# Performance work log

Hardware: AMD Instinct MI355X
Metric: run time of the kernel (lower is better)

The kernel has to match this reference:

```python
import jax, jax.numpy as jnp
import numpy as np

DN = ('NCHW', 'OIHW', 'NCHW')


def conv(x, w, s, p):
    return jax.lax.conv_general_dilated(x, w, (s, s), [(p, p), (p, p)], dimension_numbers=DN)


def batchnorm(x, g, b, eps=1e-5):
    # torch BatchNorm2d in training mode: biased batch stats over (N,H,W)
    mu = jnp.mean(x, (0, 2, 3), keepdims=True)
    var = jnp.var(x, (0, 2, 3), keepdims=True)
    return (x - mu) * jax.lax.rsqrt(var + eps) * g.reshape(1, -1, 1, 1) + b.reshape(1, -1, 1, 1)


def pconv(x, mask, W, b, s, p, gb, act):
    # PartialConvLayer.forward
    k = W.shape[-1]
    y = conv(x * mask, W, s, p)
    mc = conv(mask, jnp.ones((1, 1, k, k), x.dtype), s, p)  # all-ones mask conv (frozen)
    zero = mc == 0
    msum = jnp.where(zero, 1.0, mc)
    if b is not None:
        bias = b.reshape(1, -1, 1, 1)
        y = (y - bias) / msum + bias
    else:
        y = y / msum
    y = jnp.where(zero, 0.0, y)
    new_mask = jnp.where(zero, 0.0, 1.0).astype(x.dtype)
    if gb is not None:
        y = batchnorm(y, gb[0], gb[1])
    if act == 'relu':
        y = jax.nn.relu(y)
    elif act == 'leaky':
        y = jnp.where(y >= 0, y, 0.2 * y)
    return y, new_mask


def nlm(mask, feat, h2):
    # Vectorized batch_NLM: Nadaraya-Watson estimator between miss and bkg pixels.
    # Equivalent to the original triple loop: for each miss pixel i,
    #   out[i] = sum_j exp(-||x_i-x_j||^2/h^2) x_j / sum_j exp(-...)   over bkg j.
    # Subtracting the per-row min distance before exp is mathematically identical
    # (the factor cancels in the ratio) and numerically stable.
    bs, C, H, W = feat.shape
    N = H * W
    x = feat.transpose(0, 2, 3, 1).reshape(bs, N, C)
    bkg = mask.reshape(bs, N) > 0.5
    sq = jnp.sum(x * x, -1)  # [bs,N]
    D = jnp.maximum(sq[:, :, None] + sq[:, None, :] - 2.0 * jnp.einsum('bic,bjc->bij', x, x), 0.0)
    Dm = jnp.where(bkg[:, None, :], D, jnp.inf)
    dmin = jnp.min(Dm, -1, keepdims=True)
    w = jnp.where(bkg[:, None, :], jnp.exp(-(D - dmin) / h2), 0.0)
    avg = jnp.einsum('bij,bjc->bic', w, x) / jnp.sum(w, -1, keepdims=True)
    out = jnp.where(bkg[:, :, None], x, avg)  # only miss pixels are replaced
    return out.reshape(bs, H, W, C).transpose(0, 3, 1, 2)


def up2(x):
    return jnp.repeat(jnp.repeat(x, 2, axis=2), 2, axis=3)


def forward(input_x, mask, enc1_W, enc2_W, enc3_W, enc4_W, dec4_W, dec3_W, dec2_W, dec1_W, dec1_b,
            enc2_g, enc2_b, enc3_g, enc3_b, enc4_g, enc4_b,
            dec4_g, dec4_b, dec3_g, dec3_b, dec2_g, dec2_b):
    H_GAUSS2 = 25.0  # h_gaussian = 5
    h0, m0 = input_x, mask
    h1, m1 = pconv(h0, m0, enc1_W, None, 2, 3, None, 'relu')                 # down-7, bn=False
    h2, m2 = pconv(h1, m1, enc2_W, None, 2, 2, (enc2_g, enc2_b), 'relu')     # down-5
    # NLM feature swapping at layer 2 (torch code detaches -> stop_gradient)
    h2 = jax.lax.stop_gradient(nlm(m2, h2, H_GAUSS2))
    buffer_swapped = h2
    h3, m3 = pconv(h2, m2, enc3_W, None, 2, 1, (enc3_g, enc3_b), 'relu')     # down-3
    h4, m4 = pconv(h3, m3, enc4_W, None, 2, 1, (enc4_g, enc4_b), 'relu')     # down-3

    out, omask = h4, m4
    out, omask = up2(out), up2(omask)
    out, omask = pconv(jnp.concatenate([out, h3], 1), omask, dec4_W, None, 1, 1, (dec4_g, dec4_b), 'leaky')
    out, omask = up2(out), up2(omask)
    out, omask = pconv(jnp.concatenate([out, buffer_swapped], 1), omask, dec3_W, None, 1, 1, (dec3_g, dec3_b), 'leaky')
    out, omask = up2(out), up2(omask)
    out, omask = pconv(jnp.concatenate([out, h1], 1), omask, dec2_W, None, 1, 1, (dec2_g, dec2_b), 'leaky')
    out, omask = up2(out), up2(omask)
    out, omask = pconv(jnp.concatenate([out, h0], 1), omask, dec1_W, dec1_b, 1, 1, None, 'none')  # bn=False, bias, no act
    return out


def setup_inputs() -> dict:
    key = jax.random.key(0)
    ks = jax.random.split(key, 12)

    def kaiming(k, shape):
        fan_in = shape[1] * shape[2] * shape[3]
        return jax.random.normal(k, shape, jnp.float32) * np.float32(np.sqrt(2.0 / fan_in))

    bs = 8
    input_x = jax.random.normal(ks[0], (bs, 128, 144, 144), jnp.float32)
    # mask: 1 = background (valid), 0 = missing. Hole large enough to survive two downsamples.
    mask = jnp.ones((bs, 1, 144, 144), jnp.float32).at[:, :, 40:96, 40:96].set(0.0)

    inp = {
        'input_x': input_x,
        'mask': mask,
        'enc1_W': kaiming(ks[1], (256, 128, 7, 7)),
        'enc2_W': kaiming(ks[2], (512, 256, 5, 5)),
        'enc3_W': kaiming(ks[3], (512, 512, 3, 3)),
        'enc4_W': kaiming(ks[4], (512, 512, 3, 3)),
        'dec4_W': kaiming(ks[5], (512, 1024, 3, 3)),
        'dec3_W': kaiming(ks[6], (512, 1024, 3, 3)),
        'dec2_W': kaiming(ks[7], (256, 768, 3, 3)),
        'dec1_W': kaiming(ks[8], (128, 384, 3, 3)),
        'dec1_b': jnp.zeros((128,), jnp.float32),
    }
    for name, c in [('enc2', 512), ('enc3', 512), ('enc4', 512), ('dec4', 512), ('dec3', 512), ('dec2', 256)]:
        inp[name + '_g'] = jnp.ones((c,), jnp.float32)
        inp[name + '_b'] = jnp.zeros((c,), jnp.float32)
    return inp


def reference(input_x, mask, enc1_W, enc2_W, enc3_W, enc4_W, dec4_W, dec3_W, dec2_W, dec1_W, dec1_b,
              enc2_g, enc2_b, enc3_g, enc3_b, enc4_g, enc4_b,
              dec4_g, dec4_b, dec3_g, dec3_b, dec2_g, dec2_b):
    return forward(input_x, mask, enc1_W, enc2_W, enc3_W, enc4_W, dec4_W, dec3_W, dec2_W, dec1_W, dec1_b,
                   enc2_g, enc2_b, enc3_g, enc3_b, enc4_g, enc4_b,
                   dec4_g, dec4_b, dec3_g, dec3_b, dec2_g, dec2_b)
```

## Files before the change

### kernel.cpp

```cpp
#include <hip/hip_runtime.h>
#include <math.h>

#define ACT_NONE 0
#define ACT_RELU 1
#define ACT_LEAKY 2

#define EPI_F32 0
#define EPI_PAIR_RELU 1
#define EPI_F32_BIAS 2

typedef __attribute__((ext_vector_type(8))) short short8;
typedef __attribute__((ext_vector_type(8))) __bf16 bf16x8;
typedef __attribute__((ext_vector_type(4))) float f32x4;
typedef __attribute__((ext_vector_type(4))) unsigned uint4v;

__device__ __forceinline__ float actf(float y, int act) {
    if (act == ACT_RELU)  return y > 0.f ? y : 0.f;
    if (act == ACT_LEAKY) return y >= 0.f ? y : 0.2f * y;
    return y;
}

__device__ __forceinline__ unsigned f2bf_rne(float f) {
    unsigned u = __float_as_uint(f);
    return (u + 0x7FFFu + ((u >> 16) & 1u)) >> 16;
}
__device__ __forceinline__ float bf2f(unsigned h) { return __uint_as_float(h << 16); }
__device__ __forceinline__ unsigned splitpack(float f) {
    unsigned hi = f2bf_rne(f);
    float r = f - bf2f(hi);
    unsigned lo = f2bf_rne(r);
    return (hi & 0xFFFFu) | (lo << 16);
}

__device__ __forceinline__ f32x4 mfma16(short8 a, short8 b, f32x4 c) {
    return __builtin_amdgcn_mfma_f32_16x16x32_bf16(
        __builtin_bit_cast(bf16x8, a), __builtin_bit_cast(bf16x8, b), c, 0, 0, 0);
}

template<int K, int S, bool MHALF>
__global__ void maskconv_kernel(const float* __restrict__ M, int HM, int WM,
                                float* __restrict__ mc, float* __restrict__ nm,
                                int N, int Hin, int Win, int Hout, int Wout) {
    constexpr int P = (K - 1) / 2;
    int idx = blockIdx.x * blockDim.x + threadIdx.x;
    int total = N * Hout * Wout;
    if (idx >= total) return;
    int wo = idx % Wout;
    int t  = idx / Wout;
    int ho = t % Hout;
    int n  = t / Hout;
    float s = 0.f;
    for (int kh = 0; kh < K; ++kh) {
        int ih = ho * S - P + kh;
        if ((unsigned)ih >= (unsigned)Hin) continue;
        const float* mrow = M + ((size_t)n * HM + (MHALF ? (ih >> 1) : ih)) * WM;
        for (int kw = 0; kw < K; ++kw) {
            int iw = wo * S - P + kw;
            if ((unsigned)iw < (unsigned)Win)
                s += mrow[MHALF ? (iw >> 1) : iw];
        }
    }
    mc[idx] = s;
    nm[idx] = (s == 0.f) ? 0.f : 1.f;
}

__global__ void wtransform(const float* __restrict__ W, short* __restrict__ Whi,
                           short* __restrict__ Wlo, int Cout, int Cin, int Ksz,
                           size_t total) {
    size_t idx = (size_t)blockIdx.x * blockDim.x + threadIdx.x;
    if (idx >= total) return;
    int j = (int)(idx & 7);
    int lane = (int)((idx >> 3) & 63);
    size_t r = idx >> 9;
    int COB = Cout >> 4, KB = Cin >> 5;
    int cob = (int)(r % COB); r /= COB;
    int kb = (int)(r % KB);
    int tap = (int)(r / KB);
    int co = cob * 16 + (lane & 15);
    int ci = kb * 32 + (lane >> 4) * 8 + j;
    float f = W[((size_t)co * Cin + ci) * Ksz + tap];
    unsigned hi = f2bf_rne(f);
    float rr = f - bf2f(hi);
    unsigned lo = f2bf_rne(rr);
    Whi[idx] = (short)hi;
    Wlo[idx] = (short)lo;
}

template<int K, int S, int TH, int TW, int NFW, bool AF32, int EPI>
__global__ __launch_bounds__(512) void conv_enc(
    const void* __restrict__ Asrc, int Cin, int Hin, int Win,
    const float* __restrict__ M,
    const short* __restrict__ Whi, const short* __restrict__ Wlo,
    const float* __restrict__ mc, const float* __restrict__ bias,
    void* __restrict__ outp,
    int Hout, int Wout, int Cout, int TX)
{
    constexpr int P = (K - 1) / 2;
    constexpr int HH  = (TH - 1) * S + K;
    constexpr int HWC = (TW - 1) * S + K;
    constexpr int PXC = HH * HWC;
    __shared__ __align__(16) unsigned BH[4 * PXC * 4];
    __shared__ __align__(16) unsigned BL[4 * PXC * 4];

    const int t    = threadIdx.x;
    const int lane = t & 63;
    const int wv   = t >> 6;
    const int wm   = wv >> 1;
    const int wn   = wv & 1;
    const int img  = blockIdx.z;
    const int coB  = blockIdx.y * 256;
    const int tile = blockIdx.x;
    const int ty   = tile / TX, tx = tile - ty * TX;
    const int oy0  = ty * TH, ox0 = tx * TW;
    const int KB   = Cin >> 5;
    const int COB  = Cout >> 4;
    const size_t HW = (size_t)Hin * Win;
    const int g  = lane >> 4;
    const int pl = lane & 15;

    f32x4 acc[4][NFW] = {};

#pragma unroll 1
    for (int kb = 0; kb < KB; ++kb) {
        for (int q = t; q < PXC; q += 512) {
            const int r = q / HWC, c = q - r * HWC;
            const int iy = oy0 * S - P + r;
            const int ix = ox0 * S - P + c;
            bool sel = (unsigned)iy < (unsigned)Hin && (unsigned)ix < (unsigned)Win;
            size_t base = 0;
            if (sel) {
                sel = M[(size_t)img * HW + (size_t)iy * Win + ix] != 0.f;
                base = (size_t)img * Cin * HW + (size_t)iy * Win + ix;
            }
#pragma unroll
            for (int gg = 0; gg < 4; ++gg) {
                const int c0 = kb * 32 + gg * 8;
                unsigned v[8];
#pragma unroll
                for (int j = 0; j < 8; ++j) v[j] = 0u;
                if (sel) {
                    if (AF32) {
                        const float* s = (const float*)Asrc + base + (size_t)c0 * HW;
#pragma unroll
                        for (int j = 0; j < 8; ++j) v[j] = splitpack(s[(size_t)j * HW]);
                    } else {
                        const unsigned* s = (const unsigned*)Asrc + base + (size_t)c0 * HW;
#pragma unroll
                        for (int j = 0; j < 8; ++j) v[j] = s[(size_t)j * HW];
                    }
                }
                uint4v hd, ld;
#pragma unroll
                for (int j = 0; j < 4; ++j) {
                    hd[j] = (v[2 * j] & 0xFFFFu) | (v[2 * j + 1] << 16);
                    ld[j] = (v[2 * j] >> 16) | (v[2 * j + 1] & 0xFFFF0000u);
                }
                *(uint4v*)&BH[(gg * PXC + q) * 4] = hd;
                *(uint4v*)&BL[(gg * PXC + q) * 4] = ld;
            }
        }
        __syncthreads();

#pragma unroll 1
        for (int kh = 0; kh < K; ++kh)
#pragma unroll 1
        for (int kw = 0; kw < K; ++kw) {
            const int tap = kh * K + kw;
            const size_t wb = (((size_t)tap * KB + kb) * COB + (coB >> 4) + wm * 4) * 512
                            + (size_t)lane * 8;
            short8 ah[4], al[4];
#pragma unroll
            for (int fm = 0; fm < 4; ++fm) {
                ah[fm] = *(const short8*)(Whi + wb + (size_t)fm * 512);
                al[fm] = *(const short8*)(Wlo + wb + (size_t)fm * 512);
            }
#pragma unroll
            for (int fn = 0; fn < NFW; ++fn) {
                const int pxf = (wn * NFW + fn) * 16 + pl;
                const int oy = pxf / TW, ox = pxf - oy * TW;
                const int h = (oy * S + kh) * HWC + ox * S + kw;
                short8 bh = *(const short8*)&BH[(g * PXC + h) * 4];
                short8 bl = *(const short8*)&BL[(g * PXC + h) * 4];
#pragma unroll
                for (int fm = 0; fm < 4; ++fm) {
                    acc[fm][fn] = mfma16(ah[fm], bh, acc[fm][fn]);
                    acc[fm][fn] = mfma16(al[fm], bh, acc[fm][fn]);
                    acc[fm][fn] = mfma16(ah[fm], bl, acc[fm][fn]);
                }
            }
        }
        __syncthreads();
    }

    const int Npix = Hout * Wout;
    const float* mcb = mc + (size_t)img * Npix;
#pragma unroll
    for (int fm = 0; fm < 4; ++fm)
#pragma unroll
    for (int fn = 0; fn < NFW; ++fn) {
        const int co = coB + (wm * 4 + fm) * 16 + (lane >> 4) * 4;
        const int pxf = (wn * NFW + fn) * 16 + (lane & 15);
        const int oy = pxf / TW, ox = pxf - oy * TW;
        const int gy = oy0 + oy, gx = ox0 + ox;
        if (gy >= Hout || gx >= Wout) continue;
        const float m = mcb[(size_t)gy * Wout + gx];
        f32x4 a = acc[fm][fn];
#pragma unroll
        for (int r = 0; r < 4; ++r) {
            float y = a[r];
            if (EPI == EPI_F32_BIAS) {
                const float bv = bias[co + r];
                y = (m == 0.f) ? 0.f : (y - bv) / m + bv;
            } else {
                y = (m == 0.f) ? 0.f : y / m;
            }
            const size_t oidx = ((size_t)img * Cout + co + r) * Npix + (size_t)gy * Wout + gx;
            if (EPI == EPI_PAIR_RELU) {
                y = y > 0.f ? y : 0.f;
                ((unsigned*)outp)[oidx] = splitpack(y);
            } else {
                ((float*)outp)[oidx] = y;
            }
        }
    }
}

template<int TH, int TW, int NF, bool BF32, int EPI>
__global__ __launch_bounds__(512) void conv3x3(
    const void* __restrict__ Asrc, int CA, int HA, int WA,
    const void* __restrict__ Bsrc, int CB,
    const float* __restrict__ M,
    const short* __restrict__ Whi, const short* __restrict__ Wlo,
    const float* __restrict__ mc, const float* __restrict__ bias,
    void* __restrict__ outp,
    int Hout, int Wout, int Cout, int TX)
{
    constexpr int HALO_H = TH + 2, HALO_W = TW + 2, HALO = HALO_H * HALO_W;
    constexpr int NFW = NF / 2;
    constexpr int NPIX = TH * TW;
    __shared__ __align__(16) unsigned BH[4 * HALO * 4];
    __shared__ __align__(16) unsigned BL[4 * HALO * 4];

    const int t    = threadIdx.x;
    const int lane = t & 63;
    const int wv   = t >> 6;
    const int wm   = wv >> 1;
    const int wn   = wv & 1;
    const int img  = blockIdx.z;
    const int coB  = blockIdx.y * 128;
    const int tile = blockIdx.x;
    const int ty   = tile / TX;
    const int tx   = tile - ty * TX;
    const int oy0  = ty * TH, ox0 = tx * TW;
    const int Cin  = CA + CB;
    const int KB   = Cin >> 5;
    const int COB  = Cout >> 4;
    const int WM   = Wout >> 1;
    const size_t HWA = (size_t)HA * WA;
    const size_t HWB = (size_t)Hout * Wout;

    bool sel = false;
    size_t abase = 0, bbase = 0;
    if (t < HALO) {
        const int hy = t / HALO_W, hx = t - hy * HALO_W;
        const int iy = oy0 - 1 + hy, ix = ox0 - 1 + hx;
        if ((unsigned)iy < (unsigned)Hout && (unsigned)ix < (unsigned)Wout) {
            sel = M[((size_t)img * (Hout >> 1) + (iy >> 1)) * WM + (ix >> 1)] != 0.f;
            if (sel) {
                abase = (size_t)img * CA * HWA + (size_t)(iy >> 1) * WA + (ix >> 1);
                bbase = (size_t)img * CB * HWB + (size_t)iy * Wout + ix;
            }
        }
    }

    f32x4 acc[2][NFW] = {};
    const size_t wstride = (size_t)KB * COB * 512;

#pragma unroll 1
    for (int kb = 0; kb < KB; ++kb) {
        if (t < HALO) {
            const int ci0 = kb * 32;
#pragma unroll
            for (int g = 0; g < 4; ++g) {
                const int c = ci0 + g * 8;
                unsigned v[8];
#pragma unroll
                for (int j = 0; j < 8; ++j) v[j] = 0u;
                if (sel) {
                    if (c < CA) {
                        const unsigned* s = (const unsigned*)Asrc + abase + (size_t)c * HWA;
#pragma unroll
                        for (int j = 0; j < 8; ++j) v[j] = s[(size_t)j * HWA];
                    } else {
                        if (BF32) {
                            const float* s = (const float*)Bsrc + bbase + (size_t)(c - CA) * HWB;
#pragma unroll
                            for (int j = 0; j < 8; ++j) v[j] = splitpack(s[(size_t)j * HWB]);
                        } else {
                            const unsigned* s = (const unsigned*)Bsrc + bbase + (size_t)(c - CA) * HWB;
#pragma unroll
                            for (int j = 0; j < 8; ++j) v[j] = s[(size_t)j * HWB];
                        }
                    }
                }
                uint4v hd, ld;
#pragma unroll
                for (int j = 0; j < 4; ++j) {
                    hd[j] = (v[2 * j] & 0xFFFFu) | (v[2 * j + 1] << 16);
                    ld[j] = (v[2 * j] >> 16) | (v[2 * j + 1] & 0xFFFF0000u);
                }
                *(uint4v*)&BH[(g * HALO + t) * 4] = hd;
                *(uint4v*)&BL[(g * HALO + t) * 4] = ld;
            }
        }
        __syncthreads();

        size_t wb = ((size_t)kb * COB + (coB >> 4) + wm * 2) * 512 + lane * 8;
        short8 ah0 = *(const short8*)(Whi + wb);
        short8 ah1 = *(const short8*)(Whi + wb + 512);
        short8 al0 = *(const short8*)(Wlo + wb);
        short8 al1 = *(const short8*)(Wlo + wb + 512);

        const int g = lane >> 4;
        const int pl = lane & 15;
        int dh = 0, dw = 0;
#pragma unroll 1
        for (int tap = 0; tap < 9; ++tap) {
            const size_t wbn = wb + ((tap < 8) ? wstride : 0);
            short8 nh0 = *(const short8*)(Whi + wbn);
            short8 nh1 = *(const short8*)(Whi + wbn + 512);
            short8 nl0 = *(const short8*)(Wlo + wbn);
            short8 nl1 = *(const short8*)(Wlo + wbn + 512);

#pragma unroll
            for (int fn = 0; fn < NFW; ++fn) {
                int pxf = (wn * NFW + fn) * 16 + pl;
                pxf = pxf < NPIX ? pxf : NPIX - 1;
                const int oy = pxf / TW, ox = pxf - oy * TW;
                const int hpx = (oy + dh) * HALO_W + (ox + dw);
                short8 bh = *(const short8*)&BH[(g * HALO + hpx) * 4];
                short8 bl = *(const short8*)&BL[(g * HALO + hpx) * 4];
                acc[0][fn] = mfma16(ah0, bh, acc[0][fn]);
                acc[1][fn] = mfma16(ah1, bh, acc[1][fn]);
                acc[0][fn] = mfma16(al0, bh, acc[0][fn]);
                acc[1][fn] = mfma16(al1, bh, acc[1][fn]);
                acc[0][fn] = mfma16(ah0, bl, acc[0][fn]);
                acc[1][fn] = mfma16(ah1, bl, acc[1][fn]);
            }
            ah0 = nh0; ah1 = nh1; al0 = nl0; al1 = nl1;
            wb = wbn;
            if (++dw == 3) { dw = 0; ++dh; }
        }
        __syncthreads();
    }

    const float* mcb = mc + (size_t)img * HWB;
#pragma unroll
    for (int fm = 0; fm < 2; ++fm)
#pragma unroll
    for (int fn = 0; fn < NFW; ++fn) {
        const int co = coB + (wm * 2 + fm) * 16 + (lane >> 4) * 4;
        const int pxf = (wn * NFW + fn) * 16 + (lane & 15);
        if (pxf >= NPIX) continue;
        const int oy = pxf / TW, ox = pxf - oy * TW;
        const int gy = oy0 + oy, gx = ox0 + ox;
        if (gy >= Hout || gx >= Wout) continue;
        const float m = mcb[(size_t)gy * Wout + gx];
        f32x4 a = acc[fm][fn];
#pragma unroll
        for (int r = 0; r < 4; ++r) {
            float y = a[r];
            if (EPI == EPI_F32_BIAS) {
                const float bv = bias[co + r];
                y = (m == 0.f) ? 0.f : (y - bv) / m + bv;
            } else {
                y = (m == 0.f) ? 0.f : y / m;
            }
            ((float*)outp)[((size_t)img * Cout + co + r) * HWB + (size_t)gy * Wout + gx] = y;
        }
    }
}

__global__ __launch_bounds__(256) void bn_stats_kernel(const float* __restrict__ y,
                                                       int N, int C, int HW,
                                                       float* __restrict__ mean,
                                                       float* __restrict__ istd) {
    const int c = blockIdx.x;
    double s = 0.0, s2 = 0.0;
    const int tot = N * HW;
    for (int i = threadIdx.x; i < tot; i += blockDim.x) {
        int n = i / HW, hw = i - n * HW;
        float v = y[((size_t)n * C + c) * HW + hw];
        s += v;
        s2 += (double)v * v;
    }
    __shared__ double sh[256], sh2[256];
    sh[threadIdx.x] = s; sh2[threadIdx.x] = s2;
    __syncthreads();
    for (int o = 128; o > 0; o >>= 1) {
        if (threadIdx.x < o) { sh[threadIdx.x] += sh[threadIdx.x + o]; sh2[threadIdx.x] += sh2[threadIdx.x + o]; }
        __syncthreads();
    }
    if (threadIdx.x == 0) {
        double mu = sh[0] / tot;
        double var = sh2[0] / tot - mu * mu;
        mean[c] = (float)mu;
        istd[c] = (float)(1.0 / sqrt(var + 1e-5));
    }
}

__global__ void bn_apply_pair(const float* __restrict__ y,
                              const float* __restrict__ mean, const float* __restrict__ istd,
                              const float* __restrict__ g, const float* __restrict__ b,
                              unsigned* __restrict__ pout, float* __restrict__ fout,
                              int C, int HW, int total, int act) {
    int idx = blockIdx.x * blockDim.x + threadIdx.x;
    if (idx >= total) return;
    int c = (idx / HW) % C;
    float v = (y[idx] - mean[c]) * istd[c] * g[c] + b[c];
    v = actf(v, act);
    pout[idx] = splitpack(v);
    if (fout) fout[idx] = v;
}

#define NLM_C 512
#define NLM_N 1296
#define NLM_MAXM 256
#define NLM_RT 16
#define NLM_KB1 16
#define NLM_KB2 41
#define NLM_PFRAG (NLM_KB1 * NLM_RT * 512)
#define NLM_WFRAG (NLM_KB2 * NLM_RT * 512)

__global__ __launch_bounds__(256) void nlm_trans(const float* __restrict__ h2f,
                                                 unsigned* __restrict__ xTp) {
    __shared__ float tile[32][33];
    const int b = blockIdx.z;
    const int j0 = blockIdx.x * 32, c0 = blockIdx.y * 32;
    const int tx = threadIdx.x & 31, ty = threadIdx.x >> 5;
    for (int cc = ty; cc < 32; cc += 8) {
        const int j = j0 + tx;
        tile[cc][tx] = (j < NLM_N) ? h2f[((size_t)b * NLM_C + c0 + cc) * NLM_N + j] : 0.f;
    }
    __syncthreads();
    for (int jj = ty; jj < 32; jj += 8) {
        const int j = j0 + jj;
        if (j < NLM_N)
            xTp[((size_t)b * NLM_N + j) * NLM_C + c0 + tx] = splitpack(tile[tx][jj]);
    }
}

__global__ void nlm_sq2(const float* __restrict__ h2f, float* __restrict__ sq) {
    const int b = blockIdx.y;
    const int j = blockIdx.x * 256 + threadIdx.x;
    if (j >= NLM_N) return;
    const float* p = h2f + (size_t)b * NLM_C * NLM_N + j;
    float s0 = 0.f, s1 = 0.f, s2 = 0.f, s3 = 0.f;
    for (int c = 0; c < NLM_C; c += 4) {
        float v0 = p[(size_t)c * NLM_N];
        float v1 = p[(size_t)(c + 1) * NLM_N];
        float v2 = p[(size_t)(c + 2) * NLM_N];
        float v3 = p[(size_t)(c + 3) * NLM_N];
        s0 = fmaf(v0, v0, s0); s1 = fmaf(v1, v1, s1);
        s2 = fmaf(v2, v2, s2); s3 = fmaf(v3, v3, s3);
    }
    sq[b * NLM_N + j] = (s0 + s1) + (s2 + s3);
}

__global__ void nlm_compact(const float* __restrict__ nm2, int* __restrict__ list,
                            int* __restrict__ cnt) {
    const int b = blockIdx.x;
    for (int j = threadIdx.x; j < NLM_N; j += 256) {
        if (nm2[(size_t)b * NLM_N + j] == 0.f) {
            int pos = atomicAdd(&cnt[b], 1);
            if (pos < NLM_MAXM) list[b * NLM_MAXM + pos] = j;
        }
    }
}

__global__ void nlm_gather(const unsigned* __restrict__ xTp, const int* __restrict__ list,
                           const int* __restrict__ cnt,
                           short* __restrict__ Phi, short* __restrict__ Plo) {
    const int b = blockIdx.y;
    const int id = blockIdx.x * 256 + threadIdx.x;
    const int i  = id >> 6;
    const int rem = id & 63;
    const int kb = rem >> 2, kg = rem & 3;
    const int lane = kg * 16 + (i & 15), rt = i >> 4;
    const size_t f = (size_t)b * NLM_PFRAG + ((size_t)(kb * NLM_RT + rt) * 64 + lane) * 8;
    if (i < cnt[b]) {
        const int pix = list[b * NLM_MAXM + i];
        const unsigned* s = xTp + ((size_t)b * NLM_N + pix) * NLM_C + kb * 32 + kg * 8;
#pragma unroll
        for (int jj = 0; jj < 8; ++jj) {
            unsigned v = s[jj];
            Phi[f + jj] = (short)(v & 0xFFFFu);
            Plo[f + jj] = (short)(v >> 16);
        }
    } else {
#pragma unroll
        for (int jj = 0; jj < 8; ++jj) { Phi[f + jj] = 0; Plo[f + jj] = 0; }
    }
}

__global__ __launch_bounds__(512) void nlm_gemm1(
    const unsigned* __restrict__ xTp, const short* __restrict__ Phi,
    const short* __restrict__ Plo, const int* __restrict__ cnt,
    float* __restrict__ S) {
    const int img = blockIdx.z, mt = blockIdx.y, nt = blockIdx.x;
    if (mt * 128 >= cnt[img]) return;
    __shared__ __align__(16) unsigned BH[4 * 128 * 4];
    __shared__ __align__(16) unsigned BL[4 * 128 * 4];
    const int t = threadIdx.x, lane = t & 63, wv = t >> 6, wm = wv >> 1, wn = wv & 1;
    const int j0 = nt * 128;
    const int spx = t & 127, sg = t >> 7;
    f32x4 acc[2][4] = {};
#pragma unroll 1
    for (int kb = 0; kb < NLM_KB1; ++kb) {
        unsigned v[8];
#pragma unroll
        for (int jj = 0; jj < 8; ++jj) v[jj] = 0u;
        const int j = j0 + spx;
        if (j < NLM_N) {
            const unsigned* s = xTp + ((size_t)img * NLM_N + j) * NLM_C + kb * 32 + sg * 8;
#pragma unroll
            for (int jj = 0; jj < 8; ++jj) v[jj] = s[jj];
        }
        uint4v hd, ld;
#pragma unroll
        for (int jj = 0; jj < 4; ++jj) {
            hd[jj] = (v[2 * jj] & 0xFFFFu) | (v[2 * jj + 1] << 16);
            ld[jj] = (v[2 * jj] >> 16) | (v[2 * jj + 1] & 0xFFFF0000u);
        }
        *(uint4v*)&BH[(sg * 128 + spx) * 4] = hd;
        *(uint4v*)&BL[(sg * 128 + spx) * 4] = ld;
        __syncthreads();
        const size_t ab = (size_t)img * NLM_PFRAG
                        + (size_t)(kb * NLM_RT + mt * 8 + wm * 2) * 512 + (size_t)lane * 8;
        short8 ah0 = *(const short8*)(Phi + ab);
        short8 ah1 = *(const short8*)(Phi + ab + 512);
        short8 al0 = *(const short8*)(Plo + ab);
        short8 al1 = *(const short8*)(Plo + ab + 512);
        const int g = lane >> 4, pl = lane & 15;
#pragma unroll
        for (int fn = 0; fn < 4; ++fn) {
            const int px = wn * 64 + fn * 16 + pl;
            short8 bh = *(const short8*)&BH[(g * 128 + px) * 4];
            short8 bl = *(const short8*)&BL[(g * 128 + px) * 4];
            acc[0][fn] = mfma16(ah0, bh, acc[0][fn]);
            acc[1][fn] = mfma16(ah1, bh, acc[1][fn]);
            acc[0][fn] = mfma16(al0, bh, acc[0][fn]);
            acc[1][fn] = mfma16(al1, bh, acc[1][fn]);
            acc[0][fn] = mfma16(ah0, bl, acc[0][fn]);
            acc[1][fn] = mfma16(ah1, bl, acc[1][fn]);
        }
        __syncthreads();
    }
#pragma unroll
    for (int fm = 0; fm < 2; ++fm)
#pragma unroll
    for (int fn = 0; fn < 4; ++fn) {
        const int row = mt * 128 + (wm * 2 + fm) * 16 + (lane >> 4) * 4;
        const int j = j0 + wn * 64 + fn * 16 + (lane & 15);
        if (j >= NLM_N) continue;
        f32x4 a = acc[fm][fn];
#pragma unroll
        for (int r = 0; r < 4; ++r)
            S[((size_t)img * NLM_MAXM + row + r) * NLM_N + j] = a[r];
    }
}

__global__ __launch_bounds__(256) void nlm_row(
    const float* __restrict__ S, const float* __restrict__ sq,
    const float* __restrict__ nm2, const int* __restrict__ list,
    const int* __restrict__ cnt,
    short* __restrict__ W2hi, short* __restrict__ W2lo,
    float* __restrict__ sumw, float inv_h2) {
    const int img = blockIdx.y, i = blockIdx.x;
    if (i >= cnt[img] || i >= NLM_MAXM) return;
    __shared__ float Drow[NLM_N];
    __shared__ float red[256];
    const int tid = threadIdx.x;
    const int pix = list[img * NLM_MAXM + i];
    const float sqi = sq[img * NLM_N + pix];
    const float BIG = 3.4e38f;
    float lmin = BIG;
    for (int j = tid; j < NLM_N; j += 256) {
        float d = BIG;
        if (nm2[(size_t)img * NLM_N + j] != 0.f) {
            float dot = S[((size_t)img * NLM_MAXM + i) * NLM_N + j];
            d = sqi + sq[img * NLM_N + j] - 2.f * dot;
            d = d > 0.f ? d : 0.f;
            lmin = d < lmin ? d : lmin;
        }
        Drow[j] = d;
    }
    red[tid] = lmin;
    __syncthreads();
    for (int o = 128; o > 0; o >>= 1) {
        if (tid < o) red[tid] = fminf(red[tid], red[tid + o]);
        __syncthreads();
    }
    const float dmin = red[0];
    __syncthreads();

    const int rt = i >> 4, lr = i & 15;
    float lsum = 0.f;
    for (int j = tid; j < NLM_KB2 * 32; j += 256) {
        float w = 0.f;
        if (j < NLM_N && Drow[j] < 3.3e38f) {
            w = expf(-(Drow[j] - dmin) * inv_h2);
            lsum += w;
        }
        const unsigned u = splitpack(w);
        const int kb = j >> 5, kg = (j & 31) >> 3, jj = j & 7;
        const int lane = kg * 16 + lr;
        const size_t f = (size_t)img * NLM_WFRAG
                       + ((size_t)(kb * NLM_RT + rt) * 64 + lane) * 8 + jj;
        W2hi[f] = (short)(u & 0xFFFFu);
        W2lo[f] = (short)(u >> 16);
    }
    red[tid] = lsum;
    __syncthreads();
    for (int o = 128; o > 0; o >>= 1) {
        if (tid < o) red[tid] += red[tid + o];
        __syncthreads();
    }
    if (tid == 0) sumw[img * NLM_MAXM + i] = red[0];
}

__global__ __launch_bounds__(512) void nlm_gemm2(
    const unsigned* __restrict__ xTp, const short* __restrict__ W2hi,
    const short* __restrict__ W2lo, const int* __restrict__ cnt,
    const float* __restrict__ sumw, const int* __restrict__ list,
    unsigned* __restrict__ out) {
    const int img = blockIdx.z, mt = blockIdx.y, ct = blockIdx.x;
    const int cN = cnt[img] < NLM_MAXM ? cnt[img] : NLM_MAXM;
    if (mt * 128 >= cN) return;
    __shared__ __align__(16) unsigned BH[4 * 128 * 4];
    __shared__ __align__(16) unsigned BL[4 * 128 * 4];
    const int t = threadIdx.x, lane = t & 63, wv = t >> 6, wm = wv >> 1, wn = wv & 1;
    const int c0 = ct * 128;
    const int sc = t & 127, sg = t >> 7;
    f32x4 acc[2][4] = {};
#pragma unroll 1
    for (int kb = 0; kb < NLM_KB2; ++kb) {
        unsigned v[8];
#pragma unroll
        for (int jj = 0; jj < 8; ++jj) {
            const int j = kb * 32 + sg * 8 + jj;
            v[jj] = (j < NLM_N)
                  ? xTp[((size_t)img * NLM_N + j) * NLM_C + c0 + sc] : 0u;
        }
        uint4v hd, ld;
#pragma unroll
        for (int jj = 0; jj < 4; ++jj) {
            hd[jj] = (v[2 * jj] & 0xFFFFu) | (v[2 * jj + 1] << 16);
            ld[jj] = (v[2 * jj] >> 16) | (v[2 * jj + 1] & 0xFFFF0000u);
        }
        *(uint4v*)&BH[(sg * 128 + sc) * 4] = hd;
        *(uint4v*)&BL[(sg * 128 + sc) * 4] = ld;
        __syncthreads();
        const size_t ab = (size_t)img * NLM_WFRAG
                        + (size_t)(kb * NLM_RT + mt * 8 + wm * 2) * 512 + (size_t)lane * 8;
        short8 ah0 = *(const short8*)(W2hi + ab);
        short8 ah1 = *(const short8*)(W2hi + ab + 512);
        short8 al0 = *(const short8*)(W2lo + ab);
        short8 al1 = *(const short8*)(W2lo + ab + 512);
        const int g = lane >> 4, pl = lane & 15;
#pragma unroll
        for (int fn = 0; fn < 4; ++fn) {
            const int px = wn * 64 + fn * 16 + pl;
            short8 bh = *(const short8*)&BH[(g * 128 + px) * 4];
            short8 bl = *(const short8*)&BL[(g * 128 + px) * 4];
            acc[0][fn] = mfma16(ah0, bh, acc[0][fn]);
            acc[1][fn] = mfma16(ah1, bh, acc[1][fn]);
            acc[0][fn] = mfma16(al0, bh, acc[0][fn]);
            acc[1][fn] = mfma16(al1, bh, acc[1][fn]);
            acc[0][fn] = mfma16(ah0, bl, acc[0][fn]);
            acc[1][fn] = mfma16(ah1, bl, acc[1][fn]);
        }
        __syncthreads();
    }
#pragma unroll
    for (int fm = 0; fm < 2; ++fm)
#pragma unroll
    for (int fn = 0; fn < 4; ++fn) {
        const int row = mt * 128 + (wm * 2 + fm) * 16 + (lane >> 4) * 4;
        const int c = c0 + wn * 64 + fn * 16 + (lane & 15);
        f32x4 a = acc[fm][fn];
#pragma unroll
        for (int r = 0; r < 4; ++r) {
            const int ri = row + r;
            if (ri < cN) {
                const float y = a[r] / sumw[img * NLM_MAXM + ri];
                out[((size_t)img * NLM_C + c) * NLM_N + list[img * NLM_MAXM + ri]]
                    = splitpack(y);
            }
        }
    }
}

extern "C" void kernel_launch(void* const* d_in, const int* in_sizes, int n_in,
                              void* d_out, int out_size, void* d_ws, size_t ws_size,
                              hipStream_t stream) {
    const float* x0    = (const float*)d_in[0];
    const float* m0    = (const float*)d_in[1];
    const float* Wsrc[8] = {
        (const float*)d_in[2], (const float*)d_in[3], (const float*)d_in[4],
        (const float*)d_in[5], (const float*)d_in[6], (const float*)d_in[7],
        (const float*)d_in[8], (const float*)d_in[9]
    };
    const float* dec1b = (const float*)d_in[10];
    const float* enc2g = (const float*)d_in[11];
    const float* enc2b = (const float*)d_in[12];
    const float* enc3g = (const float*)d_in[13];
    const float* enc3b = (const float*)d_in[14];
    const float* enc4g = (const float*)d_in[15];
    const float* enc4b = (const float*)d_in[16];
    const float* dec4g = (const float*)d_in[17];
    const float* dec4b = (const float*)d_in[18];
    const float* dec3g = (const float*)d_in[19];
    const float* dec3b = (const float*)d_in[20];
    const float* dec2g = (const float*)d_in[21];
    const float* dec2b = (const float*)d_in[22];
    float* outp = (float*)d_out;

    const int N = 8;
    float* ws = (float*)d_ws;
    size_t off = 0;
    auto alloc = [&](size_t nf) {
        size_t o = off;
        off += ((nf + 63) / 64) * 64;
        return ws + o;
    };

    unsigned* h1pair  = (unsigned*)alloc(10616832);
    unsigned* h2spair = (unsigned*)alloc(5308416);
    unsigned* h3pair  = (unsigned*)alloc(1327104);
    unsigned* h4pair  = (unsigned*)alloc(331776);
    unsigned* d4pair  = (unsigned*)alloc(1327104);
    float* ybuf = alloc(10616832);
    float* h2f  = alloc(5308416);
    unsigned* xTp = (unsigned*)alloc(5308416);
    float* sqb  = alloc(10368);
    float* mc   = alloc(165888);
    float* nm1  = alloc(41472);
    float* nm2  = alloc(10368);
    float* nm3  = alloc(2592);
    float* nm4  = alloc(648);
    float* nmd4 = alloc(2592);
    float* nmd3 = alloc(10368);
    float* nmd2 = alloc(41472);
    float* nmx  = alloc(165888);
    float* bmean = alloc(512);
    float* bistd = alloc(512);
    short* Whi = (short*)alloc(10625024);
    short* Wlo = (short*)alloc(10625024);
    float* Smat = alloc((size_t)8 * NLM_MAXM * NLM_N);
    short* Phi  = (short*)alloc((size_t)8 * NLM_PFRAG / 2);
    short* Plo  = (short*)alloc((size_t)8 * NLM_PFRAG / 2);
    short* W2hi = (short*)alloc((size_t)8 * NLM_WFRAG / 2);
    short* W2lo = (short*)alloc((size_t)8 * NLM_WFRAG / 2);
    int*   mlist = (int*)alloc(8 * NLM_MAXM);
    int*   mcnt  = (int*)alloc(64);
    float* sumw  = alloc(8 * NLM_MAXM);
    unsigned* d3pair = h2spair;
    unsigned* d2pair = h1pair;

    if (ws_size < off * sizeof(float)) return;

    auto cdiv = [](size_t a, size_t b) { return (int)((a + b - 1) / b); };

    struct WLay { int Cout, Cin, K; size_t ofs; };
    const WLay WL[8] = {
        {256, 128, 7, 0},
        {512, 256, 5, 1605632},
        {512, 512, 3, 4882432},
        {512, 512, 3, 7241728},
        {512, 1024, 3, 9601024},
        {512, 1024, 3, 14319616},
        {256, 768, 3, 19038208},
        {128, 384, 3, 20807680},
    };
    for (int i = 0; i < 8; ++i) {
        size_t tot = (size_t)WL[i].Cout * WL[i].Cin * WL[i].K * WL[i].K;
        wtransform<<<cdiv(tot, 256), 256, 0, stream>>>(
            Wsrc[i], Whi + WL[i].ofs, Wlo + WL[i].ofs, WL[i].Cout, WL[i].Cin,
            WL[i].K * WL[i].K, tot);
    }

    maskconv_kernel<7, 2, false><<<cdiv(N * 72 * 72, 256), 256, 0, stream>>>(
        m0, 144, 144, mc, nm1, N, 144, 144, 72, 72);
    conv_enc<7, 2, 8, 8, 2, true, EPI_PAIR_RELU><<<dim3(81, 1, N), 512, 0, stream>>>(
        x0, 128, 144, 144, m0,
        Whi + WL[0].ofs, Wlo + WL[0].ofs, mc, nullptr, h1pair,
        72, 72, 256, 9);

    maskconv_kernel<5, 2, false><<<cdiv(N * 36 * 36, 256), 256, 0, stream>>>(
        nm1, 72, 72, mc, nm2, N, 72, 72, 36, 36);
    conv_enc<5, 2, 8, 8, 2, false, EPI_F32><<<dim3(25, 2, N), 512, 0, stream>>>(
        h1pair, 256, 72, 72, nm1,
        Whi + WL[1].ofs, Wlo + WL[1].ofs, mc, nullptr, ybuf,
        36, 36, 512, 5);
    bn_stats_kernel<<<512, 256, 0, stream>>>(ybuf, N, 512, 1296, bmean, bistd);
    bn_apply_pair<<<cdiv(5308416, 256), 256, 0, stream>>>(
        ybuf, bmean, bistd, enc2g, enc2b, h2spair, h2f, 512, 1296, 5308416, ACT_RELU);

    nlm_trans<<<dim3(41, 16, N), 256, 0, stream>>>(h2f, xTp);
    nlm_sq2<<<dim3(6, N), 256, 0, stream>>>(h2f, sqb);
    hipMemsetAsync(mcnt, 0, 8 * sizeof(int), stream);
    nlm_compact<<<N, 256, 0, stream>>>(nm2, mlist, mcnt);
    nlm_gather<<<dim3(64, N), 256, 0, stream>>>(xTp, mlist, mcnt, Phi, Plo);
    nlm_gemm1<<<dim3(11, 2, N), 512, 0, stream>>>(xTp, Phi, Plo, mcnt, Smat);
    nlm_row<<<dim3(NLM_MAXM, N), 256, 0, stream>>>(Smat, sqb, nm2, mlist, mcnt,
                                                   W2hi, W2lo, sumw, 1.f / 25.f);
    nlm_gemm2<<<dim3(4, 2, N), 512, 0, stream>>>(xTp, W2hi, W2lo, mcnt, sumw,
                                                 mlist, h2spair);

    maskconv_kernel<3, 2, false><<<cdiv(N * 18 * 18, 256), 256, 0, stream>>>(
        nm2, 36, 36, mc, nm3, N, 36, 36, 18, 18);
    conv_enc<3, 2, 4, 8, 1, false, EPI_F32><<<dim3(15, 2, N), 512, 0, stream>>>(
        h2spair, 512, 36, 36, nm2,
        Whi + WL[2].ofs, Wlo + WL[2].ofs, mc, nullptr, ybuf,
        18, 18, 512, 3);
    bn_stats_kernel<<<512, 256, 0, stream>>>(ybuf, N, 512, 324, bmean, bistd);
    bn_apply_pair<<<cdiv(1327104, 256), 256, 0, stream>>>(
        ybuf, bmean, bistd, enc3g, enc3b, h3pair, nullptr, 512, 324, 1327104, ACT_RELU);

    maskconv_kernel<3, 2, false><<<cdiv(N * 9 * 9, 256), 256, 0, stream>>>(
        nm3, 18, 18, mc, nm4, N, 18, 18, 9, 9);
    conv_enc<3, 2, 4, 8, 1, false, EPI_F32><<<dim3(6, 2, N), 512, 0, stream>>>(
        h3pair, 512, 18, 18, nm3,
        Whi + WL[3].ofs, Wlo + WL[3].ofs, mc, nullptr, ybuf,
        9, 9, 512, 2);
    bn_stats_kernel<<<512, 256, 0, stream>>>(ybuf, N, 512, 81, bmean, bistd);
    bn_apply_pair<<<cdiv(331776, 256), 256, 0, stream>>>(
        ybuf, bmean, bistd, enc4g, enc4b, h4pair, nullptr, 512, 81, 331776, ACT_RELU);

    maskconv_kernel<3, 1, true><<<cdiv(N * 18 * 18, 256), 256, 0, stream>>>(
        nm4, 9, 9, mc, nmd4, N, 18, 18, 18, 18);
    conv3x3<9, 6, 4, false, EPI_F32><<<dim3(6, 4, N), 512, 0, stream>>>(
        h4pair, 512, 9, 9, h3pair, 512, nm4,
        Whi + WL[4].ofs, Wlo + WL[4].ofs, mc, nullptr, ybuf,
        18, 18, 512, 3);
    bn_stats_kernel<<<512, 256, 0, stream>>>(ybuf, N, 512, 324, bmean, bistd);
    bn_apply_pair<<<cdiv(1327104, 256), 256, 0, stream>>>(
        ybuf, bmean, bistd, dec4g, dec4b, d4pair, nullptr, 512, 324, 1327104, ACT_LEAKY);

    maskconv_kernel<3, 1, true><<<cdiv(N * 36 * 36, 256), 256, 0, stream>>>(
        nmd4, 18, 18, mc, nmd3, N, 36, 36, 36, 36);
    conv3x3<12, 8, 6, false, EPI_F32><<<dim3(15, 4, N), 512, 0, stream>>>(
        d4pair, 512, 18, 18, h2spair, 512, nmd4,
        Whi + WL[5].ofs, Wlo + WL[5].ofs, mc, nullptr, ybuf,
        36, 36, 512, 5);
    bn_stats_kernel<<<512, 256, 0, stream>>>(ybuf, N, 512, 1296, bmean, bistd);
    bn_apply_pair<<<cdiv(5308416, 256), 256, 0, stream>>>(
        ybuf, bmean, bistd, dec3g, dec3b, d3pair, nullptr, 512, 1296, 5308416, ACT_LEAKY);

    maskconv_kernel<3, 1, true><<<cdiv(N * 72 * 72, 256), 256, 0, stream>>>(
        nmd3, 36, 36, mc, nmd2, N, 72, 72, 72, 72);
    conv3x3<8, 12, 6, false, EPI_F32><<<dim3(54, 2, N), 512, 0, stream>>>(
        d3pair, 512, 36, 36, h1pair, 256, nmd3,
        Whi + WL[6].ofs, Wlo + WL[6].ofs, mc, nullptr, ybuf,
        72, 72, 256, 6);
    bn_stats_kernel<<<256, 256, 0, stream>>>(ybuf, N, 256, 5184, bmean, bistd);
    bn_apply_pair<<<cdiv(10616832, 256), 256, 0, stream>>>(
        ybuf, bmean, bistd, dec2g, dec2b, d2pair, nullptr, 256, 5184, 10616832, ACT_LEAKY);

    maskconv_kernel<3, 1, true><<<cdiv(N * 144 * 144, 256), 256, 0, stream>>>(
        nmd2, 72, 72, mc, nmx, N, 144, 144, 144, 144);
    conv3x3<16, 16, 16, true, EPI_F32_BIAS><<<dim3(81, 1, N), 512, 0, stream>>>(
        d2pair, 256, 72, 72, x0, 128, nmd2,
        Whi + WL[7].ofs, Wlo + WL[7].ofs, mc, dec1b, outp,
        144, 144, 128, 9);
}
```

Baseline: 2.836 ms.

## Rework conv3x3 warp tiling to 4x64 fragments and parity-split encoder LDS layout

```diff
diff --git a/kernel.cpp b/kernel.cpp
--- a/kernel.cpp
+++ b/kernel.cpp
@@ -95,12 +95,15 @@
     void* __restrict__ outp,
     int Hout, int Wout, int Cout, int TX)
 {
+    static_assert(S == 2, "parity layout assumes stride 2");
     constexpr int P = (K - 1) / 2;
     constexpr int HH  = (TH - 1) * S + K;
     constexpr int HWC = (TW - 1) * S + K;
     constexpr int PXC = HH * HWC;
-    __shared__ __align__(16) unsigned BH[4 * PXC * 4];
-    __shared__ __align__(16) unsigned BL[4 * PXC * 4];
+    constexpr int PW  = (HWC + 1) / 2;
+    constexpr int PXC2 = HH * PW * 2;
+    __shared__ __align__(16) unsigned BH[4 * PXC2 * 4];
+    __shared__ __align__(16) unsigned BL[4 * PXC2 * 4];
 
     const int t    = threadIdx.x;
     const int lane = t & 63;
@@ -124,6 +127,7 @@
     for (int kb = 0; kb < KB; ++kb) {
         for (int q = t; q < PXC; q += 512) {
             const int r = q / HWC, c = q - r * HWC;
+            const int qq = r * PW + (c >> 1) + (c & 1) * (HH * PW);
             const int iy = oy0 * S - P + r;
             const int ix = ox0 * S - P + c;
             bool sel = (unsigned)iy < (unsigned)Hin && (unsigned)ix < (unsigned)Win;
@@ -155,8 +159,8 @@
                     hd[j] = (v[2 * j] & 0xFFFFu) | (v[2 * j + 1] << 16);
                     ld[j] = (v[2 * j] >> 16) | (v[2 * j + 1] & 0xFFFF0000u);
                 }
-                *(uint4v*)&BH[(gg * PXC + q) * 4] = hd;
-                *(uint4v*)&BL[(gg * PXC + q) * 4] = ld;
+                *(uint4v*)&BH[(gg * PXC2 + qq) * 4] = hd;
+                *(uint4v*)&BL[(gg * PXC2 + qq) * 4] = ld;
             }
         }
         __syncthreads();
@@ -178,9 +182,9 @@
             for (int fn = 0; fn < NFW; ++fn) {
                 const int pxf = (wn * NFW + fn) * 16 + pl;
                 const int oy = pxf / TW, ox = pxf - oy * TW;
-                const int h = (oy * S + kh) * HWC + ox * S + kw;
-                short8 bh = *(const short8*)&BH[(g * PXC + h) * 4];
-                short8 bl = *(const short8*)&BL[(g * PXC + h) * 4];
+                const int qq = (oy * S + kh) * PW + ox + (kw >> 1) + (kw & 1) * (HH * PW);
+                short8 bh = *(const short8*)&BH[(g * PXC2 + qq) * 4];
+                short8 bl = *(const short8*)&BL[(g * PXC2 + qq) * 4];
 #pragma unroll
                 for (int fm = 0; fm < 4; ++fm) {
                     acc[fm][fn] = mfma16(ah[fm], bh, acc[fm][fn]);
@@ -225,7 +229,7 @@
     }
 }
 
-template<int TH, int TW, int NF, bool BF32, int EPI>
+template<int TH, int TW, int NFW, bool BF32, int EPI>
 __global__ __launch_bounds__(512) void conv3x3(
     const void* __restrict__ Asrc, int CA, int HA, int WA,
     const void* __restrict__ Bsrc, int CB,
@@ -236,16 +240,16 @@
     int Hout, int Wout, int Cout, int TX)
 {
     constexpr int HALO_H = TH + 2, HALO_W = TW + 2, HALO = HALO_H * HALO_W;
-    constexpr int NFW = NF / 2;
     constexpr int NPIX = TH * TW;
+    static_assert(NPIX == 64 * NFW, "tile must be 64*NFW pixels");
     __shared__ __align__(16) unsigned BH[4 * HALO * 4];
     __shared__ __align__(16) unsigned BL[4 * HALO * 4];
 
     const int t    = threadIdx.x;
     const int lane = t & 63;
     const int wv   = t >> 6;
-    const int wm   = wv >> 1;
-    const int wn   = wv & 1;
+    const int wm   = wv & 1;
+    const int wn   = wv >> 1;
     const int img  = blockIdx.z;
     const int coB  = blockIdx.y * 128;
     const int tile = blockIdx.x;
@@ -259,109 +263,96 @@
     const size_t HWA = (size_t)HA * WA;
     const size_t HWB = (size_t)Hout * Wout;
 
-    bool sel = false;
-    size_t abase = 0, bbase = 0;
-    if (t < HALO) {
-        const int hy = t / HALO_W, hx = t - hy * HALO_W;
-        const int iy = oy0 - 1 + hy, ix = ox0 - 1 + hx;
-        if ((unsigned)iy < (unsigned)Hout && (unsigned)ix < (unsigned)Wout) {
-            sel = M[((size_t)img * (Hout >> 1) + (iy >> 1)) * WM + (ix >> 1)] != 0.f;
-            if (sel) {
-                abase = (size_t)img * CA * HWA + (size_t)(iy >> 1) * WA + (ix >> 1);
-                bbase = (size_t)img * CB * HWB + (size_t)iy * Wout + ix;
-            }
-        }
-    }
-
-    f32x4 acc[2][NFW] = {};
+    const int sg = t >> 7;
+    const int st = t & 127;
+    const int g  = lane >> 4;
+    const int pl = lane & 15;
+
+    f32x4 acc[4][NFW] = {};
     const size_t wstride = (size_t)KB * COB * 512;
 
 #pragma unroll 1
     for (int kb = 0; kb < KB; ++kb) {
-        if (t < HALO) {
-            const int ci0 = kb * 32;
-#pragma unroll
-            for (int g = 0; g < 4; ++g) {
-                const int c = ci0 + g * 8;
-                unsigned v[8];
-#pragma unroll
-                for (int j = 0; j < 8; ++j) v[j] = 0u;
+        for (int q = st; q < HALO; q += 128) {
+            const int hy = q / HALO_W, hx = q - hy * HALO_W;
+            const int iy = oy0 - 1 + hy, ix = ox0 - 1 + hx;
+            bool sel = false;
+            size_t abase = 0, bbase = 0;
+            if ((unsigned)iy < (unsigned)Hout && (unsigned)ix < (unsigned)Wout) {
+                sel = M[((size_t)img * (Hout >> 1) + (iy >> 1)) * WM + (ix >> 1)] != 0.f;
                 if (sel) {
-                    if (c < CA) {
-                        const unsigned* s = (const unsigned*)Asrc + abase + (size_t)c * HWA;
-#pragma unroll
-                        for (int j = 0; j < 8; ++j) v[j] = s[(size_t)j * HWA];
+                    abase = (size_t)img * CA * HWA + (size_t)(iy >> 1) * WA + (ix >> 1);
+                    bbase = (size_t)img * CB * HWB + (size_t)iy * Wout + ix;
+                }
+            }
+            const int c = kb * 32 + sg * 8;
+            unsigned v[8];
+#pragma unroll
+            for (int j = 0; j < 8; ++j) v[j] = 0u;
+            if (sel) {
+                if (c < CA) {
+                    const unsigned* s = (const unsigned*)Asrc + abase + (size_t)c * HWA;
+#pragma unroll
+                    for (int j = 0; j < 8; ++j) v[j] = s[(size_t)j * HWA];
+                } else {
+                    if (BF32) {
+                        const float* s = (const float*)Bsrc + bbase + (size_t)(c - CA) * HWB;
+#pragma unroll
+                        for (int j = 0; j < 8; ++j) v[j] = splitpack(s[(size_t)j * HWB]);
                     } else {
-                        if (BF32) {
-                            const float* s = (const float*)Bsrc + bbase + (size_t)(c - CA) * HWB;
-#pragma unroll
-                            for (int j = 0; j < 8; ++j) v[j] = splitpack(s[(size_t)j * HWB]);
-                        } else {
-                            const unsigned* s = (const unsigned*)Bsrc + bbase + (size_t)(c - CA) * HWB;
-#pragma unroll
-                            for (int j = 0; j < 8; ++j) v[j] = s[(size_t)j * HWB];
-                        }
+                        const unsigned* s = (const unsigned*)Bsrc + bbase + (size_t)(c - CA) * HWB;
+#pragma unroll
+                        for (int j = 0; j < 8; ++j) v[j] = s[(size_t)j * HWB];
                     }
                 }
-                uint4v hd, ld;
-#pragma unroll
-                for (int j = 0; j < 4; ++j) {
-                    hd[j] = (v[2 * j] & 0xFFFFu) | (v[2 * j + 1] << 16);
-                    ld[j] = (v[2 * j] >> 16) | (v[2 * j + 1] & 0xFFFF0000u);
-                }
-                *(uint4v*)&BH[(g * HALO + t) * 4] = hd;
-                *(uint4v*)&BL[(g * HALO + t) * 4] = ld;
-            }
-        }
-        __syncthreads();
-
-        size_t wb = ((size_t)kb * COB + (coB >> 4) + wm * 2) * 512 + lane * 8;
-        short8 ah0 = *(const short8*)(Whi + wb);
-        short8 ah1 = *(const short8*)(Whi + wb + 512);
-        short8 al0 = *(const short8*)(Wlo + wb);
-        short8 al1 = *(const short8*)(Wlo + wb + 512);
-
-        const int g = lane >> 4;
-        const int pl = lane & 15;
-        int dh = 0, dw = 0;
+            }
+            uint4v hd, ld;
+#pragma unroll
+            for (int j = 0; j < 4; ++j) {
+                hd[j] = (v[2 * j] & 0xFFFFu) | (v[2 * j + 1] << 16);
+                ld[j] = (v[2 * j] >> 16) | (v[2 * j + 1] & 0xFFFF0000u);
+            }
+            *(uint4v*)&BH[(sg * HALO + q) * 4] = hd;
+            *(uint4v*)&BL[(sg * HALO + q) * 4] = ld;
+        }
+        __syncthreads();
+
+        size_t wb = ((size_t)kb * COB + (coB >> 4) + wm * 4) * 512 + (size_t)lane * 8;
 #pragma unroll 1
         for (int tap = 0; tap < 9; ++tap) {
-            const size_t wbn = wb + ((tap < 8) ? wstride : 0);
-            short8 nh0 = *(const short8*)(Whi + wbn);
-            short8 nh1 = *(const short8*)(Whi + wbn + 512);
-            short8 nl0 = *(const short8*)(Wlo + wbn);
-            short8 nl1 = *(const short8*)(Wlo + wbn + 512);
-
+            const int dh = tap / 3, dw = tap - dh * 3;
+            short8 ah[4], al[4];
+#pragma unroll
+            for (int fm = 0; fm < 4; ++fm) {
+                ah[fm] = *(const short8*)(Whi + wb + (size_t)fm * 512);
+                al[fm] = *(const short8*)(Wlo + wb + (size_t)fm * 512);
+            }
 #pragma unroll
             for (int fn = 0; fn < NFW; ++fn) {
-                int pxf = (wn * NFW + fn) * 16 + pl;
-                pxf = pxf < NPIX ? pxf : NPIX - 1;
+                const int pxf = (wn * NFW + fn) * 16 + pl;
                 const int oy = pxf / TW, ox = pxf - oy * TW;
                 const int hpx = (oy + dh) * HALO_W + (ox + dw);
                 short8 bh = *(const short8*)&BH[(g * HALO + hpx) * 4];
                 short8 bl = *(const short8*)&BL[(g * HALO + hpx) * 4];
-                acc[0][fn] = mfma16(ah0, bh, acc[0][fn]);
-                acc[1][fn] = mfma16(ah1, bh, acc[1][fn]);
-                acc[0][fn] = mfma16(al0, bh, acc[0][fn]);
-                acc[1][fn] = mfma16(al1, bh, acc[1][fn]);
-                acc[0][fn] = mfma16(ah0, bl, acc[0][fn]);
-                acc[1][fn] = mfma16(ah1, bl, acc[1][fn]);
-            }
-            ah0 = nh0; ah1 = nh1; al0 = nl0; al1 = nl1;
-            wb = wbn;
-            if (++dw == 3) { dw = 0; ++dh; }
+#pragma unroll
+                for (int fm = 0; fm < 4; ++fm) {
+                    acc[fm][fn] = mfma16(ah[fm], bh, acc[fm][fn]);
+                    acc[fm][fn] = mfma16(al[fm], bh, acc[fm][fn]);
+                    acc[fm][fn] = mfma16(ah[fm], bl, acc[fm][fn]);
+                }
+            }
+            wb += wstride;
         }
         __syncthreads();
     }
 
     const float* mcb = mc + (size_t)img * HWB;
 #pragma unroll
-    for (int fm = 0; fm < 2; ++fm)
+    for (int fm = 0; fm < 4; ++fm)
 #pragma unroll
     for (int fn = 0; fn < NFW; ++fn) {
-        const int co = coB + (wm * 2 + fm) * 16 + (lane >> 4) * 4;
+        const int co = coB + (wm * 4 + fm) * 16 + (lane >> 4) * 4;
         const int pxf = (wn * NFW + fn) * 16 + (lane & 15);
-        if (pxf >= NPIX) continue;
         const int oy = pxf / TW, ox = pxf - oy * TW;
         const int gy = oy0 + oy, gx = ox0 + ox;
         if (gy >= Hout || gx >= Wout) continue;
@@ -840,7 +831,7 @@
 
     maskconv_kernel<3, 1, true><<<cdiv(N * 18 * 18, 256), 256, 0, stream>>>(
         nm4, 9, 9, mc, nmd4, N, 18, 18, 18, 18);
-    conv3x3<9, 6, 4, false, EPI_F32><<<dim3(6, 4, N), 512, 0, stream>>>(
+    conv3x3<8, 8, 1, false, EPI_F32><<<dim3(9, 4, N), 512, 0, stream>>>(
         h4pair, 512, 9, 9, h3pair, 512, nm4,
         Whi + WL[4].ofs, Wlo + WL[4].ofs, mc, nullptr, ybuf,
         18, 18, 512, 3);
@@ -850,27 +841,27 @@
 
     maskconv_kernel<3, 1, true><<<cdiv(N * 36 * 36, 256), 256, 0, stream>>>(
         nmd4, 18, 18, mc, nmd3, N, 36, 36, 36, 36);
-    conv3x3<12, 8, 6, false, EPI_F32><<<dim3(15, 4, N), 512, 0, stream>>>(
+    conv3x3<12, 16, 3, false, EPI_F32><<<dim3(9, 4, N), 512, 0, stream>>>(
         d4pair, 512, 18, 18, h2spair, 512, nmd4,
         Whi + WL[5].ofs, Wlo + WL[5].ofs, mc, nullptr, ybuf,
-        36, 36, 512, 5);
+        36, 36, 512, 3);
     bn_stats_kernel<<<512, 256, 0, stream>>>(ybuf, N, 512, 1296, bmean, bistd);
     bn_apply_pair<<<cdiv(5308416, 256), 256, 0, stream>>>(
         ybuf, bmean, bistd, dec3g, dec3b, d3pair, nullptr, 512, 1296, 5308416, ACT_LEAKY);
 
     maskconv_kernel<3, 1, true><<<cdiv(N * 72 * 72, 256), 256, 0, stream>>>(
         nmd3, 36, 36, mc, nmd2, N, 72, 72, 72, 72);
-    conv3x3<8, 12, 6, false, EPI_F32><<<dim3(54, 2, N), 512, 0, stream>>>(
+    conv3x3<8, 16, 2, false, EPI_F32><<<dim3(45, 2, N), 512, 0, stream>>>(
         d3pair, 512, 36, 36, h1pair, 256, nmd3,
         Whi + WL[6].ofs, Wlo + WL[6].ofs, mc, nullptr, ybuf,
-        72, 72, 256, 6);
+        72, 72, 256, 5);
     bn_stats_kernel<<<256, 256, 0, stream>>>(ybuf, N, 256, 5184, bmean, bistd);
     bn_apply_pair<<<cdiv(10616832, 256), 256, 0, stream>>>(
         ybuf, bmean, bistd, dec2g, dec2b, d2pair, nullptr, 256, 5184, 10616832, ACT_LEAKY);
 
     maskconv_kernel<3, 1, true><<<cdiv(N * 144 * 144, 256), 256, 0, stream>>>(
         nmd2, 72, 72, mc, nmx, N, 144, 144, 144, 144);
-    conv3x3<16, 16, 16, true, EPI_F32_BIAS><<<dim3(81, 1, N), 512, 0, stream>>>(
+    conv3x3<16, 16, 4, true, EPI_F32_BIAS><<<dim3(81, 1, N), 512, 0, stream>>>(
         d2pair, 256, 72, 72, x0, 128, nmd2,
         Whi + WL[7].ofs, Wlo + WL[7].ofs, mc, dec1b, outp,
         144, 144, 128, 9);
```

Measured after the change: 3.031 ms. 1.07x slower.
